# Kernel optimization log

Hardware: AMD Instinct MI355X
Metric: run time of the kernel (lower is better)

Reference implementation:

```python
import jax, jax.numpy as jnp
import numpy as np

N = 50000      # nodes
E = 640000     # edges (before self-loops)
FIN = 512      # in_channels
H = 4          # heads
C = 32         # per-head dim (hidden_channels // heads)
HID = 128      # hidden_channels
OUT = 64       # out_channels
NC = 2         # num_classes


def setup_inputs() -> dict:
    key = jax.random.key(0)
    ks = jax.random.split(key, 26)
    rn = lambda k, shp, s=0.05: jax.random.normal(k, shp, jnp.float32) * s
    return {
        "x": jax.random.normal(ks[0], (N, FIN), jnp.float32),
        "edge_index": jax.random.randint(ks[1], (2, E), 0, N, dtype=jnp.int32),
        "batch": jnp.zeros((N,), jnp.int32),
        # GATConv 1: FIN -> H x C (concat -> HID)
        "W1": rn(ks[2], (FIN, H * C)), "as1": rn(ks[3], (H, C)), "ad1": rn(ks[4], (H, C)), "b1": jnp.zeros((H * C,), jnp.float32),
        "g1": jnp.ones((HID,), jnp.float32), "be1": jnp.zeros((HID,), jnp.float32),
        # GATConv 2: HID -> H x C
        "W2": rn(ks[5], (HID, H * C)), "as2": rn(ks[6], (H, C)), "ad2": rn(ks[7], (H, C)), "b2": jnp.zeros((H * C,), jnp.float32),
        "g2": jnp.ones((HID,), jnp.float32), "be2": jnp.zeros((HID,), jnp.float32),
        "W3": rn(ks[8], (HID, OUT)), "as3": rn(ks[9], (1, OUT)), "ad3": rn(ks[10], (1, OUT)), "b3": jnp.zeros((OUT,), jnp.float32),
        "g3": jnp.ones((OUT,), jnp.float32), "be3": jnp.zeros((OUT,), jnp.float32),
        # classifier: Linear(2*OUT, HID) -> ReLU -> Linear(HID, NC)
        "cW1": rn(ks[11], (2 * OUT, HID)), "cb1": jnp.zeros((HID,), jnp.float32),
        "cW2": rn(ks[12], (HID, NC)), "cb2": jnp.zeros((NC,), jnp.float32),
    }


def _gat_conv(x, ei, W, a_s, a_d, b, heads, cdim, concat):
    n = x.shape[0]
    h = (x @ W).reshape(n, heads, cdim)                 # [n,H,C]
    src, dst = ei[0], ei[1]
    al_s = (h * a_s).sum(-1)                            # [n,H]
    al_d = (h * a_d).sum(-1)                            # [n,H]
    e = al_s[src] + al_d[dst]                           # [E',H]
    e = jnp.where(e > 0, e, 0.2 * e)                    # LeakyReLU(0.2)
    m = jax.ops.segment_max(e, dst, num_segments=n)     # segment softmax over dst
    ex = jnp.exp(e - m[dst])
    s = jax.ops.segment_sum(ex, dst, num_segments=n)
    alpha = ex / (s[dst] + 1e-16)                       # [E',H]
    out = jax.ops.segment_sum(h[src] * alpha[:, :, None], dst, num_segments=n)
    out = out.reshape(n, heads * cdim) if concat else out.mean(axis=1)
    return out + b


def _layer_norm(x, g, b):
    mu = x.mean(-1, keepdims=True)
    v = ((x - mu) ** 2).mean(-1, keepdims=True)
    return g * (x - mu) * jax.lax.rsqrt(v + 1e-5) + b


def reference(x, edge_index, batch, W1, as1, ad1, b1, g1, be1, W2, as2, ad2, b2, g2, be2, W3, as3, ad3, b3, g3, be3, cW1, cb1, cW2, cb2):
    n = x.shape[0]
    ar = jnp.arange(n, dtype=edge_index.dtype)
    ei = jnp.concatenate([edge_index, jnp.stack([ar, ar])], axis=1)  # add self-loops (PyG default)
    h = jax.nn.elu(_layer_norm(_gat_conv(x, ei, W1, as1, ad1, b1, H, C, True), g1, be1))
    h = jax.nn.elu(_layer_norm(_gat_conv(h, ei, W2, as2, ad2, b2, H, C, True), g2, be2))
    h = jax.nn.elu(_layer_norm(_gat_conv(h, ei, W3, as3, ad3, b3, 1, OUT, False), g3, be3))
    # global mean / max pooling over batch ids (single graph here, B=1)
    B = 1
    cnt = jax.ops.segment_sum(jnp.ones((n, 1), h.dtype), batch, num_segments=B)
    x_mean = jax.ops.segment_sum(h, batch, num_segments=B) / cnt
    x_max = jax.ops.segment_max(h, batch, num_segments=B)
    z = jnp.concatenate([x_mean, x_max], axis=-1)       # [B, 2*OUT]
    z = jax.nn.relu(z @ cW1 + cb1)
    return z @ cW2 + cb2                                 # [B, NC]
```

## Files before the change

### kernel.cpp

```cpp
#include <hip/hip_runtime.h>
#include <cmath>

static constexpr int TPB = 256;

using short8 = __attribute__((ext_vector_type(8))) short;
using half8  = __attribute__((ext_vector_type(8))) _Float16;
using f32x4  = __attribute__((ext_vector_type(4))) float;
using uint4v = __attribute__((ext_vector_type(4))) unsigned int;
typedef unsigned short ushort;
typedef unsigned int uint;

__device__ __forceinline__ ushort f2h(float f) {
  _Float16 h = (_Float16)f;
  return __builtin_bit_cast(ushort, h);
}
__device__ __forceinline__ float h2f(ushort u) {
  return (float)__builtin_bit_cast(_Float16, u);
}
__device__ __forceinline__ float hlo(uint u) { return h2f((ushort)(u & 0xffffu)); }
__device__ __forceinline__ float hhi(uint u) { return h2f((ushort)(u >> 16)); }

__global__ void prep_wt3(const float* __restrict__ W1, ushort* __restrict__ Wt1,
                         const float* __restrict__ W2, ushort* __restrict__ Wt2,
                         const float* __restrict__ W3, ushort* __restrict__ Wt3,
                         int FIN) {
  int idx = blockIdx.x * TPB + threadIdx.x;
  const int n1 = FIN * 128, n2 = 128 * 128, n3 = 128 * 64;
  if (idx < n1) {
    int nc = idx / FIN, k = idx - nc * FIN;
    Wt1[idx] = f2h(W1[(size_t)k * 128 + nc]);
  } else if (idx < n1 + n2) {
    int i = idx - n1;
    int nc = i / 128, k = i - nc * 128;
    Wt2[i] = f2h(W2[(size_t)k * 128 + nc]);
  } else if (idx < n1 + n2 + n3) {
    int i = idx - n1 - n2;
    int nc = i / 128, k = i - nc * 128;
    Wt3[i] = f2h(W3[(size_t)k * 64 + nc]);
  }
}

template <int ABF16, int BN, bool FUSE>
__global__ __launch_bounds__(256) void gemm_mfma(const void* __restrict__ Ap,
                                                 const ushort* __restrict__ Wt,
                                                 ushort* __restrict__ Cb,
                                                 int n, int K,
                                                 const float* __restrict__ a_s,
                                                 const float* __restrict__ a_d,
                                                 float* __restrict__ als,
                                                 float* __restrict__ ald) {
  constexpr int NF = BN / 32;
  __shared__ short As[64 * 72];
  __shared__ short Bs[BN * 72];
  const int tid = threadIdx.x;
  const int row0 = blockIdx.x * 64;
  const int srow = tid >> 2, sks = (tid & 3) << 4;
  const int wave = tid >> 6, lane = tid & 63;
  const int wr = wave >> 1, wc = wave & 1;
  const int lm = lane & 15, lg = lane >> 4;

  f32x4 acc[2][NF] = {};

  for (int k0 = 0; k0 < K; k0 += 64) {
    {
      int gr = row0 + srow;
      short8 v0 = {0, 0, 0, 0, 0, 0, 0, 0}, v1 = v0;
      if constexpr (ABF16 == 0) {
        const float* A = (const float*)Ap;
        if (gr < n) {
          const float* p = A + (size_t)gr * K + k0 + sks;
          float4 f0 = *(const float4*)(p + 0);
          float4 f1 = *(const float4*)(p + 4);
          float4 f2 = *(const float4*)(p + 8);
          float4 f3 = *(const float4*)(p + 12);
          v0[0] = (short)f2h(f0.x); v0[1] = (short)f2h(f0.y); v0[2] = (short)f2h(f0.z); v0[3] = (short)f2h(f0.w);
          v0[4] = (short)f2h(f1.x); v0[5] = (short)f2h(f1.y); v0[6] = (short)f2h(f1.z); v0[7] = (short)f2h(f1.w);
          v1[0] = (short)f2h(f2.x); v1[1] = (short)f2h(f2.y); v1[2] = (short)f2h(f2.z); v1[3] = (short)f2h(f2.w);
          v1[4] = (short)f2h(f3.x); v1[5] = (short)f2h(f3.y); v1[6] = (short)f2h(f3.z); v1[7] = (short)f2h(f3.w);
        }
      } else {
        const ushort* A = (const ushort*)Ap;
        if (gr < n) {
          const ushort* p = A + (size_t)gr * K + k0 + sks;
          v0 = *(const short8*)(p + 0);
          v1 = *(const short8*)(p + 8);
        }
      }
      *(short8*)&As[srow * 72 + sks + 0] = v0;
      *(short8*)&As[srow * 72 + sks + 8] = v1;
    }
    if constexpr (BN == 128) {
      const int brow = tid >> 1, bks = (tid & 1) << 5;
      const ushort* wp = Wt + (size_t)brow * K + k0 + bks;
      *(short8*)&Bs[brow * 72 + bks + 0]  = *(const short8*)(wp + 0);
      *(short8*)&Bs[brow * 72 + bks + 8]  = *(const short8*)(wp + 8);
      *(short8*)&Bs[brow * 72 + bks + 16] = *(const short8*)(wp + 16);
      *(short8*)&Bs[brow * 72 + bks + 24] = *(const short8*)(wp + 24);
    } else {
      const ushort* wp = Wt + (size_t)srow * K + k0 + sks;
      *(short8*)&Bs[srow * 72 + sks + 0] = *(const short8*)(wp + 0);
      *(short8*)&Bs[srow * 72 + sks + 8] = *(const short8*)(wp + 8);
    }
    __syncthreads();
#pragma unroll
    for (int kk = 0; kk < 64; kk += 32) {
      half8 a0 = *(const half8*)&As[(wr * 32 + lm) * 72 + kk + lg * 8];
      half8 a1 = *(const half8*)&As[(wr * 32 + 16 + lm) * 72 + kk + lg * 8];
      half8 bf[NF];
#pragma unroll
      for (int f = 0; f < NF; ++f)
        bf[f] = *(const half8*)&Bs[(wc * (BN / 2) + f * 16 + lm) * 72 + kk + lg * 8];
#pragma unroll
      for (int f = 0; f < NF; ++f) {
        acc[0][f] = __builtin_amdgcn_mfma_f32_16x16x32_f16(a0, bf[f], acc[0][f], 0, 0, 0);
        acc[1][f] = __builtin_amdgcn_mfma_f32_16x16x32_f16(a1, bf[f], acc[1][f], 0, 0, 0);
      }
    }
    __syncthreads();
  }
#pragma unroll
  for (int m = 0; m < 2; ++m)
#pragma unroll
    for (int f = 0; f < NF; ++f)
#pragma unroll
      for (int r = 0; r < 4; ++r) {
        int row = row0 + wr * 32 + m * 16 + lg * 4 + r;
        if (row < n) {
          int col = wc * (BN / 2) + f * 16 + lm;
          Cb[(size_t)row * BN + col] = f2h(acc[m][f][r]);
        }
      }
  if constexpr (FUSE) {
#pragma unroll
    for (int hh = 0; hh < 2; ++hh) {
      const int head = 2 * wc + hh;
      float as0 = a_s[head * 32 + lm], as1 = a_s[head * 32 + 16 + lm];
      float ad0 = a_d[head * 32 + lm], ad1 = a_d[head * 32 + 16 + lm];
#pragma unroll
      for (int m = 0; m < 2; ++m)
#pragma unroll
        for (int r = 0; r < 4; ++r) {
          float tS = acc[m][2 * hh][r] * as0 + acc[m][2 * hh + 1][r] * as1;
          float tD = acc[m][2 * hh][r] * ad0 + acc[m][2 * hh + 1][r] * ad1;
#pragma unroll
          for (int off = 8; off >= 1; off >>= 1) {
            tS += __shfl_xor(tS, off);
            tD += __shfl_xor(tD, off);
          }
          if (lm == 0) {
            int row = row0 + wr * 32 + m * 16 + lg * 4 + r;
            if (row < n) {
              als[(size_t)row * 4 + head] = tS;
              ald[(size_t)row * 4 + head] = tD;
            }
          }
        }
    }
  }
}

template <int HH, int CC>
__global__ void compute_al(const ushort* __restrict__ hb, const float* __restrict__ a_s,
                           const float* __restrict__ a_d, float* __restrict__ als,
                           float* __restrict__ ald, int n) {
  int idx = blockIdx.x * TPB + threadIdx.x;
  if (idx >= n * HH) return;
  int node = idx / HH, h = idx - (idx / HH) * HH;
  const ushort* hp = hb + (size_t)node * (HH * CC) + h * CC;
  float s = 0.f, d = 0.f;
#pragma unroll
  for (int c8 = 0; c8 < CC; c8 += 8) {
    short8 v = *(const short8*)(hp + c8);
#pragma unroll
    for (int j = 0; j < 8; ++j) {
      float f = h2f((ushort)v[j]);
      s += f * a_s[h * CC + c8 + j];
      d += f * a_d[h * CC + c8 + j];
    }
  }
  als[idx] = s;
  ald[idx] = d;
}

__global__ void zero_int(int* __restrict__ p, int n) {
  int i = blockIdx.x * TPB + threadIdx.x;
  if (i < n) p[i] = 0;
}

__global__ void hist_dst(const int* __restrict__ edst, int* __restrict__ counts,
                         int E0, int Et) {
  int e = blockIdx.x * TPB + threadIdx.x;
  if (e >= Et) return;
  int d = e < E0 ? edst[e] : e - E0;
  atomicAdd(&counts[d], 1);
}

__global__ void block_sums(const int* __restrict__ counts, int* __restrict__ bsum, int N) {
  __shared__ int sh[256];
  int t = threadIdx.x, idx = blockIdx.x * 256 + t;
  sh[t] = idx < N ? counts[idx] : 0;
  __syncthreads();
  for (int off = 128; off >= 1; off >>= 1) {
    if (t < off) sh[t] += sh[t + off];
    __syncthreads();
  }
  if (t == 0) bsum[blockIdx.x] = sh[0];
}

__global__ void scan_bsum(int* __restrict__ bsum, int nb) {
  __shared__ int sh[256];
  int t = threadIdx.x;
  int v = t < nb ? bsum[t] : 0;
  sh[t] = v;
  __syncthreads();
  for (int off = 1; off < 256; off <<= 1) {
    int u = (t >= off) ? sh[t - off] : 0;
    __syncthreads();
    sh[t] += u;
    __syncthreads();
  }
  if (t < nb) bsum[t] = sh[t] - v;
}

__global__ void scan_final(const int* __restrict__ counts, const int* __restrict__ bsum_ex,
                           int* __restrict__ offsets, int* __restrict__ cursor,
                           int N, int Et) {
  __shared__ int sh[256];
  int t = threadIdx.x, b = blockIdx.x;
  int idx = b * 256 + t;
  int v = (idx < N) ? counts[idx] : 0;
  sh[t] = v;
  __syncthreads();
  for (int off = 1; off < 256; off <<= 1) {
    int u = (t >= off) ? sh[t - off] : 0;
    __syncthreads();
    sh[t] += u;
    __syncthreads();
  }
  if (idx < N) {
    int o = bsum_ex[b] + sh[t] - v;
    offsets[idx] = o;
    cursor[idx] = o;
  }
  if (idx == 0) offsets[N] = Et;
}

__global__ void scatter_csr(const int* __restrict__ esrc, const int* __restrict__ edst,
                            int* __restrict__ cursor, int* __restrict__ csr_src,
                            int E0, int Et) {
  int e = blockIdx.x * TPB + threadIdx.x;
  if (e >= Et) return;
  int s = e < E0 ? esrc[e] : e - E0;
  int d = e < E0 ? edst[e] : e - E0;
  int pos = atomicAdd(&cursor[d], 1);
  csr_src[pos] = s;
}

template <int HH, int CC>
__global__ __launch_bounds__(256) void fused_attn(
    const ushort* __restrict__ hb, const float* __restrict__ als,
    const float* __restrict__ ald, const int* __restrict__ offsets,
    const int* __restrict__ csr_src, const float* __restrict__ bias,
    const float* __restrict__ g, const float* __restrict__ be,
    ushort* __restrict__ xout, int n) {
  constexpr int W = HH * CC;
  constexpr int LPE = W / 8;
  constexpr int NEG = 64 / LPE;
  int wid = (int)((blockIdx.x * (size_t)blockDim.x + threadIdx.x) >> 6);
  int lane = threadIdx.x & 63;
  if (wid >= n) return;
  const int d = wid;
  const int begin = offsets[d], end = offsets[d + 1];
  const int deg = end - begin;

  const int grp = lane / LPE, sub = lane % LPE;
  const int c0 = sub * 8;

  float acc[8] = {};

  if (HH == 4 && deg <= 16) {
    const int h16 = lane >> 4, j16 = lane & 15;
    bool act = j16 < deg;
    int s_e = csr_src[begin + (act ? j16 : 0)];
    float e;
    {
      float ad_h = ald[(size_t)d * 4 + h16];
      e = act ? (als[(size_t)s_e * 4 + h16] + ad_h) : -1e30f;
      e = e > 0.f ? e : 0.2f * e;
    }
    float m = e;
#pragma unroll
    for (int off = 8; off >= 1; off >>= 1) m = fmaxf(m, __shfl_xor(m, off));
    float p = act ? __expf(e - m) : 0.f;
    float s = p;
#pragma unroll
    for (int off = 8; off >= 1; off >>= 1) s += __shfl_xor(s, off);
    float alpha = p / (s + 1e-16f);

    const int hc = sub >> 2;
    int j = grp;
    int sj = __shfl(s_e, j & 15);
    uint4v u = *(const uint4v*)(hb + (size_t)sj * W + c0);
    for (int j0 = 0; j0 < deg; j0 += NEG) {
      uint4v ucur = u;
      int jcur = j;
      j += NEG;
      if (j0 + NEG < deg) {
        int sn = __shfl(s_e, j & 15);
        u = *(const uint4v*)(hb + (size_t)sn * W + c0);
      }
      float w = __shfl(alpha, (hc << 4) | (jcur & 15));
#pragma unroll
      for (int i = 0; i < 4; ++i) {
        acc[2 * i]     = fmaf(w, hlo(ucur[i]), acc[2 * i]);
        acc[2 * i + 1] = fmaf(w, hhi(ucur[i]), acc[2 * i + 1]);
      }
    }
  } else {

  const int hsel = sub >> 2;
  float aldv[HH];
  if constexpr (HH == 4) {
    float4 t = *(const float4*)(ald + (size_t)d * 4);
    aldv[0] = t.x; aldv[1] = t.y; aldv[2] = t.z; aldv[3] = t.w;
  } else {
    aldv[0] = ald[d];
  }

  auto sel4 = [&](float x0, float x1, float x2, float x3) {
    float lo = (hsel & 1) ? x1 : x0;
    float hi = (hsel & 1) ? x3 : x2;
    return (hsel & 2) ? hi : lo;
  };

  if (deg <= 64) {
    bool act = lane < deg;
    int s_e = act ? csr_src[begin + lane] : 0;
    float e0 = -1e30f, e1 = -1e30f, e2 = -1e30f, e3 = -1e30f;
    if constexpr (HH == 4) {
      if (act) {
        float4 t = *(const float4*)(als + (size_t)s_e * 4);
        e0 = t.x + aldv[0]; e0 = e0 > 0.f ? e0 : 0.2f * e0;
        e1 = t.y + aldv[1]; e1 = e1 > 0.f ? e1 : 0.2f * e1;
        e2 = t.z + aldv[2]; e2 = e2 > 0.f ? e2 : 0.2f * e2;
        e3 = t.w + aldv[3]; e3 = e3 > 0.f ? e3 : 0.2f * e3;
      }
    } else {
      if (act) {
        e0 = als[s_e] + aldv[0]; e0 = e0 > 0.f ? e0 : 0.2f * e0;
      }
    }
    float m0 = e0, m1 = e1, m2 = e2, m3 = e3;
#pragma unroll
    for (int off = 32; off >= 1; off >>= 1) {
      m0 = fmaxf(m0, __shfl_xor(m0, off));
      if constexpr (HH == 4) {
        m1 = fmaxf(m1, __shfl_xor(m1, off));
        m2 = fmaxf(m2, __shfl_xor(m2, off));
        m3 = fmaxf(m3, __shfl_xor(m3, off));
      }
    }
    float p0 = act ? __expf(e0 - m0) : 0.f;
    float p1 = 0.f, p2 = 0.f, p3 = 0.f;
    if constexpr (HH == 4) {
      p1 = act ? __expf(e1 - m1) : 0.f;
      p2 = act ? __expf(e2 - m2) : 0.f;
      p3 = act ? __expf(e3 - m3) : 0.f;
    }
    float s0 = p0, s1 = p1, s2 = p2, s3 = p3;
#pragma unroll
    for (int off = 32; off >= 1; off >>= 1) {
      s0 += __shfl_xor(s0, off);
      if constexpr (HH == 4) {
        s1 += __shfl_xor(s1, off);
        s2 += __shfl_xor(s2, off);
        s3 += __shfl_xor(s3, off);
      }
    }
    float a0 = p0 / (s0 + 1e-16f);
    float a1 = 0.f, a2 = 0.f, a3 = 0.f;
    if constexpr (HH == 4) {
      a1 = p1 / (s1 + 1e-16f);
      a2 = p2 / (s2 + 1e-16f);
      a3 = p3 / (s3 + 1e-16f);
    }

    int j = grp;
    int sj = __shfl(s_e, j < 64 ? j : 0);
    uint4v u = *(const uint4v*)(hb + (size_t)sj * W + c0);
    for (int j0 = 0; j0 < deg; j0 += NEG) {
      uint4v ucur = u;
      int jcur = j;
      j += NEG;
      if (j0 + NEG < deg) {
        int sn = __shfl(s_e, j < 64 ? j : 0);
        u = *(const uint4v*)(hb + (size_t)sn * W + c0);
      }
      int jc = jcur < 64 ? jcur : 0;
      float w;
      if constexpr (HH == 4) {
        float wa = __shfl(a0, jc), wb = __shfl(a1, jc), wcx = __shfl(a2, jc), wd = __shfl(a3, jc);
        w = sel4(wa, wb, wcx, wd);
      } else {
        w = __shfl(a0, jc);
      }
      if (jcur >= deg) w = 0.f;
#pragma unroll
      for (int i = 0; i < 4; ++i) {
        acc[2 * i]     = fmaf(w, hlo(ucur[i]), acc[2 * i]);
        acc[2 * i + 1] = fmaf(w, hhi(ucur[i]), acc[2 * i + 1]);
      }
    }
  } else {
    float me[HH];
#pragma unroll
    for (int h = 0; h < HH; ++h) me[h] = -1e30f;
    for (int k = begin + lane; k < end; k += 64) {
      int s = csr_src[k];
      if constexpr (HH == 4) {
        float4 t = *(const float4*)(als + (size_t)s * 4);
        float e0 = t.x + aldv[0]; e0 = e0 > 0.f ? e0 : 0.2f * e0; me[0] = fmaxf(me[0], e0);
        float e1 = t.y + aldv[1]; e1 = e1 > 0.f ? e1 : 0.2f * e1; me[1] = fmaxf(me[1], e1);
        float e2 = t.z + aldv[2]; e2 = e2 > 0.f ? e2 : 0.2f * e2; me[2] = fmaxf(me[2], e2);
        float e3 = t.w + aldv[3]; e3 = e3 > 0.f ? e3 : 0.2f * e3; me[3] = fmaxf(me[3], e3);
      } else {
        float e0 = als[s] + aldv[0]; e0 = e0 > 0.f ? e0 : 0.2f * e0; me[0] = fmaxf(me[0], e0);
      }
    }
#pragma unroll
    for (int off = 32; off >= 1; off >>= 1)
#pragma unroll
      for (int h = 0; h < HH; ++h) me[h] = fmaxf(me[h], __shfl_xor(me[h], off));
    float se[HH];
#pragma unroll
    for (int h = 0; h < HH; ++h) se[h] = 0.f;
    for (int k = begin + lane; k < end; k += 64) {
      int s = csr_src[k];
      if constexpr (HH == 4) {
        float4 t = *(const float4*)(als + (size_t)s * 4);
        float e0 = t.x + aldv[0]; e0 = e0 > 0.f ? e0 : 0.2f * e0; se[0] += __expf(e0 - me[0]);
        float e1 = t.y + aldv[1]; e1 = e1 > 0.f ? e1 : 0.2f * e1; se[1] += __expf(e1 - me[1]);
        float e2 = t.z + aldv[2]; e2 = e2 > 0.f ? e2 : 0.2f * e2; se[2] += __expf(e2 - me[2]);
        float e3 = t.w + aldv[3]; e3 = e3 > 0.f ? e3 : 0.2f * e3; se[3] += __expf(e3 - me[3]);
      } else {
        float e0 = als[s] + aldv[0]; e0 = e0 > 0.f ? e0 : 0.2f * e0; se[0] += __expf(e0 - me[0]);
      }
    }
#pragma unroll
    for (int off = 32; off >= 1; off >>= 1)
#pragma unroll
      for (int h = 0; h < HH; ++h) se[h] += __shfl_xor(se[h], off);
    float inv[HH];
#pragma unroll
    for (int h = 0; h < HH; ++h) inv[h] = 1.f / (se[h] + 1e-16f);

    float m_my, i_my, ad_my;
    if constexpr (HH == 4) {
      m_my = sel4(me[0], me[1], me[2], me[3]);
      i_my = sel4(inv[0], inv[1], inv[2], inv[3]);
      ad_my = sel4(aldv[0], aldv[1], aldv[2], aldv[3]);
    } else {
      m_my = me[0]; i_my = inv[0]; ad_my = aldv[0];
    }
    for (int j0 = 0; j0 < deg; j0 += NEG) {
      int j = j0 + grp;
      if (j < deg) {
        int s = csr_src[begin + j];
        float as_my;
        if constexpr (HH == 4) {
          float4 t = *(const float4*)(als + (size_t)s * 4);
          as_my = sel4(t.x, t.y, t.z, t.w);
        } else {
          as_my = als[s];
        }
        float e = as_my + ad_my; e = e > 0.f ? e : 0.2f * e;
        float w = __expf(e - m_my) * i_my;
        uint4v u = *(const uint4v*)(hb + (size_t)s * W + c0);
#pragma unroll
        for (int i = 0; i < 4; ++i) {
          acc[2 * i]     = fmaf(w, hlo(u[i]), acc[2 * i]);
          acc[2 * i + 1] = fmaf(w, hhi(u[i]), acc[2 * i + 1]);
        }
      }
    }
  }
  }

#pragma unroll
  for (int i = 0; i < 8; ++i) {
    if constexpr (HH == 1) acc[i] += __shfl_xor(acc[i], 8);
    acc[i] += __shfl_xor(acc[i], 16);
    acc[i] += __shfl_xor(acc[i], 32);
  }

  float4 bv0 = *(const float4*)(bias + c0);
  float4 bv1 = *(const float4*)(bias + c0 + 4);
  float v[8];
  v[0] = acc[0] + bv0.x; v[1] = acc[1] + bv0.y; v[2] = acc[2] + bv0.z; v[3] = acc[3] + bv0.w;
  v[4] = acc[4] + bv1.x; v[5] = acc[5] + bv1.y; v[6] = acc[6] + bv1.z; v[7] = acc[7] + bv1.w;
  float sm = 0.f, s2 = 0.f;
#pragma unroll
  for (int i = 0; i < 8; ++i) { sm += v[i]; s2 += v[i] * v[i]; }
  constexpr int TOPOFF = LPE / 2;
#pragma unroll
  for (int off = TOPOFF; off >= 1; off >>= 1) {
    sm += __shfl_xor(sm, off);
    s2 += __shfl_xor(s2, off);
  }
  const float invW = 1.0f / W;
  float mu = sm * invW;
  float var = s2 * invW - mu * mu;
  float r = rsqrtf(var + 1e-5f);
  float4 gv0 = *(const float4*)(g + c0);
  float4 gv1 = *(const float4*)(g + c0 + 4);
  float4 be0 = *(const float4*)(be + c0);
  float4 be1 = *(const float4*)(be + c0 + 4);
  float gg[8] = {gv0.x, gv0.y, gv0.z, gv0.w, gv1.x, gv1.y, gv1.z, gv1.w};
  float bb[8] = {be0.x, be0.y, be0.z, be0.w, be1.x, be1.y, be1.z, be1.w};
  uint4v pk;
#pragma unroll
  for (int i = 0; i < 4; ++i) {
    float y0 = gg[2 * i] * (v[2 * i] - mu) * r + bb[2 * i];
    y0 = y0 > 0.f ? y0 : __expf(y0) - 1.f;
    float y1 = gg[2 * i + 1] * (v[2 * i + 1] - mu) * r + bb[2 * i + 1];
    y1 = y1 > 0.f ? y1 : __expf(y1) - 1.f;
    pk[i] = (uint)f2h(y0) | ((uint)f2h(y1) << 16);
  }
  if (grp == 0)
    *(uint4v*)(xout + (size_t)wid * W + c0) = pk;
}

__global__ void pool_partial(const ushort* __restrict__ h, float* __restrict__ psum,
                             float* __restrict__ pmax, int n) {
  int tid = threadIdx.x;
  float lsum = 0.f, lmax = -1e30f;
  for (size_t idx = (size_t)blockIdx.x * 256 + tid; idx < (size_t)n * 64;
       idx += (size_t)gridDim.x * 256) {
    float v = h2f(h[idx]);
    lsum += v;
    lmax = fmaxf(lmax, v);
  }
  __shared__ float ss[256], sm[256];
  ss[tid] = lsum; sm[tid] = lmax;
  __syncthreads();
  if (tid < 64) {
    float a = ss[tid] + ss[tid + 64] + ss[tid + 128] + ss[tid + 192];
    float m = fmaxf(fmaxf(sm[tid], sm[tid + 64]), fmaxf(sm[tid + 128], sm[tid + 192]));
    psum[blockIdx.x * 64 + tid] = a;
    pmax[blockIdx.x * 64 + tid] = m;
  }
}

__global__ __launch_bounds__(256) void pool_final(
    const float* __restrict__ psum, const float* __restrict__ pmax,
    int nblocks, int n, const float* __restrict__ cW1,
    const float* __restrict__ cb1, const float* __restrict__ cW2,
    const float* __restrict__ cb2, float* __restrict__ out) {
  __shared__ float sred[4][64], mred[4][64];
  __shared__ float z[128];
  __shared__ float hid[128];
  int tid = threadIdx.x;
  int c = tid & 63, q = tid >> 6;
  float s = 0.f, m = -1e30f;
  for (int b = q; b < nblocks; b += 4) {
    s += psum[b * 64 + c];
    m = fmaxf(m, pmax[b * 64 + c]);
  }
  sred[q][c] = s; mred[q][c] = m;
  __syncthreads();
  if (q == 0) {
    float st = sred[0][c] + sred[1][c] + sred[2][c] + sred[3][c];
    float mt = fmaxf(fmaxf(mred[0][c], mred[1][c]), fmaxf(mred[2][c], mred[3][c]));
    z[c] = st / (float)n;
    z[64 + c] = mt;
  }
  __syncthreads();
  if (tid < 128) {
    float a = cb1[tid];
#pragma unroll 4
    for (int k = 0; k < 128; ++k) a += z[k] * cW1[k * 128 + tid];
    hid[tid] = fmaxf(a, 0.f);
  }
  __syncthreads();
  if (tid < 2) {
    float o = cb2[tid];
    for (int j = 0; j < 128; ++j) o += hid[j] * cW2[j * 2 + tid];
    out[tid] = o;
  }
}

static inline int cdiv(long long a, long long b) { return (int)((a + b - 1) / b); }

extern "C" void kernel_launch(void* const* d_in, const int* in_sizes, int n_in,
                              void* d_out, int out_size, void* d_ws, size_t ws_size,
                              hipStream_t stream) {
  const float* x   = (const float*)d_in[0];
  const int*   ei  = (const int*)d_in[1];
  const float* W1  = (const float*)d_in[3];
  const float* as1 = (const float*)d_in[4];
  const float* ad1 = (const float*)d_in[5];
  const float* b1  = (const float*)d_in[6];
  const float* g1  = (const float*)d_in[7];
  const float* be1 = (const float*)d_in[8];
  const float* W2  = (const float*)d_in[9];
  const float* as2 = (const float*)d_in[10];
  const float* ad2 = (const float*)d_in[11];
  const float* b2  = (const float*)d_in[12];
  const float* g2  = (const float*)d_in[13];
  const float* be2 = (const float*)d_in[14];
  const float* W3  = (const float*)d_in[15];
  const float* as3 = (const float*)d_in[16];
  const float* ad3 = (const float*)d_in[17];
  const float* b3  = (const float*)d_in[18];
  const float* g3  = (const float*)d_in[19];
  const float* be3 = (const float*)d_in[20];
  const float* cW1 = (const float*)d_in[21];
  const float* cb1 = (const float*)d_in[22];
  const float* cW2 = (const float*)d_in[23];
  const float* cb2 = (const float*)d_in[24];
  float* out = (float*)d_out;

  const int N   = in_sizes[2];
  const int E0  = in_sizes[1] / 2;
  const int Et  = E0 + N;
  const int FIN = in_sizes[0] / N;

  float* ws = (float*)d_ws;
  size_t o = 0;
  ushort* Ab = (ushort*)(ws + o); o += (size_t)N * 64;
  ushort* Bb = (ushort*)(ws + o); o += (size_t)N * 64;
  float* als  = ws + o; o += (size_t)N * 4;
  float* ald  = ws + o; o += (size_t)N * 4;
  ushort* Wt1 = (ushort*)(ws + o); o += (128 * 512) / 2;
  ushort* Wt2 = (ushort*)(ws + o); o += (128 * 128) / 2;
  ushort* Wt3 = (ushort*)(ws + o); o += (64 * 128) / 2;
  float* psum = ws + o; o += 64 * 64;
  float* pmax = ws + o; o += 64 * 64;
  int* counts  = (int*)(ws + o); o += N + 1;
  int* offsets = (int*)(ws + o); o += N + 1;
  int* cursor  = (int*)(ws + o); o += N;
  int* bsum    = (int*)(ws + o); o += 256;
  int* csr_src = (int*)(ws + o); o += Et;

  const int* esrc = ei;
  const int* edst = ei + E0;
  const int NB = cdiv(N, 256);

  prep_wt3<<<cdiv((long long)FIN * 128 + 128 * 128 + 128 * 64, TPB), TPB, 0, stream>>>(
      W1, Wt1, W2, Wt2, W3, Wt3, FIN);

  zero_int<<<cdiv(N + 1, TPB), TPB, 0, stream>>>(counts, N + 1);
  hist_dst<<<cdiv(Et, TPB), TPB, 0, stream>>>(edst, counts, E0, Et);
  block_sums<<<NB, 256, 0, stream>>>(counts, bsum, N);
  scan_bsum<<<1, 256, 0, stream>>>(bsum, NB);
  scan_final<<<NB, 256, 0, stream>>>(counts, bsum, offsets, cursor, N, Et);
  scatter_csr<<<cdiv(Et, TPB), TPB, 0, stream>>>(esrc, edst, cursor, csr_src, E0, Et);

  gemm_mfma<0, 128, true><<<cdiv(N, 64), 256, 0, stream>>>(x, Wt1, Ab, N, FIN, as1, ad1, als, ald);
  fused_attn<4, 32><<<cdiv(N, 4), 256, 0, stream>>>(Ab, als, ald, offsets, csr_src, b1, g1, be1, Bb, N);
  gemm_mfma<1, 128, true><<<cdiv(N, 64), 256, 0, stream>>>(Bb, Wt2, Ab, N, 128, as2, ad2, als, ald);
  fused_attn<4, 32><<<cdiv(N, 4), 256, 0, stream>>>(Ab, als, ald, offsets, csr_src, b2, g2, be2, Bb, N);
  gemm_mfma<1, 64, false><<<cdiv(N, 64), 256, 0, stream>>>(Bb, Wt3, Ab, N, 128, nullptr, nullptr, nullptr, nullptr);
  compute_al<1, 64><<<cdiv((long long)N, TPB), TPB, 0, stream>>>(Ab, as3, ad3, als, ald, N);
  fused_attn<1, 64><<<cdiv(N, 4), 256, 0, stream>>>(Ab, als, ald, offsets, csr_src, b3, g3, be3, Bb, N);
  pool_partial<<<64, 256, 0, stream>>>(Bb, psum, pmax, N);
  pool_final<<<1, 256, 0, stream>>>(psum, pmax, 64, N, cW1, cb1, cW2, cb2, out);
}
```

Measured before the change: 321.3 us.

## Prefetch next GEMM tile into registers and batch neighbor gathers in aggregation

The MFMA GEMM now loads the next K-tile from global memory into registers while the current tile is being multiplied, then writes it to shared memory between two barriers. The edge aggregation loops replace a one-ahead prefetch with four independent gathers per step, giving more memory loads in flight. Together these aim to hide global-memory latency in both the GEMM and the gather-heavy aggregation. The cost is higher register pressure, an extra barrier per K-step, and predicated or wasted work when a node's degree is not a multiple of the batch size.

Result: slower. 380.6 us (+18.5%).

```diff
diff --git a/kernel.cpp b/kernel.cpp
--- a/kernel.cpp
+++ b/kernel.cpp
@@ -55,53 +55,73 @@
   const int tid = threadIdx.x;
   const int row0 = blockIdx.x * 64;
   const int srow = tid >> 2, sks = (tid & 3) << 4;
+  const int brow = tid >> 1, bks = (tid & 1) << 5;
   const int wave = tid >> 6, lane = tid & 63;
   const int wr = wave >> 1, wc = wave & 1;
   const int lm = lane & 15, lg = lane >> 4;
 
   f32x4 acc[2][NF] = {};
 
-  for (int k0 = 0; k0 < K; k0 += 64) {
-    {
-      int gr = row0 + srow;
-      short8 v0 = {0, 0, 0, 0, 0, 0, 0, 0}, v1 = v0;
-      if constexpr (ABF16 == 0) {
-        const float* A = (const float*)Ap;
-        if (gr < n) {
-          const float* p = A + (size_t)gr * K + k0 + sks;
-          float4 f0 = *(const float4*)(p + 0);
-          float4 f1 = *(const float4*)(p + 4);
-          float4 f2 = *(const float4*)(p + 8);
-          float4 f3 = *(const float4*)(p + 12);
-          v0[0] = (short)f2h(f0.x); v0[1] = (short)f2h(f0.y); v0[2] = (short)f2h(f0.z); v0[3] = (short)f2h(f0.w);
-          v0[4] = (short)f2h(f1.x); v0[5] = (short)f2h(f1.y); v0[6] = (short)f2h(f1.z); v0[7] = (short)f2h(f1.w);
-          v1[0] = (short)f2h(f2.x); v1[1] = (short)f2h(f2.y); v1[2] = (short)f2h(f2.z); v1[3] = (short)f2h(f2.w);
-          v1[4] = (short)f2h(f3.x); v1[5] = (short)f2h(f3.y); v1[6] = (short)f2h(f3.z); v1[7] = (short)f2h(f3.w);
-        }
-      } else {
-        const ushort* A = (const ushort*)Ap;
-        if (gr < n) {
-          const ushort* p = A + (size_t)gr * K + k0 + sks;
-          v0 = *(const short8*)(p + 0);
-          v1 = *(const short8*)(p + 8);
-        }
-      }
-      *(short8*)&As[srow * 72 + sks + 0] = v0;
-      *(short8*)&As[srow * 72 + sks + 8] = v1;
+  short8 sa0, sa1;
+  short8 sb0, sb1, sb2, sb3;
+
+  auto LOADT = [&](int k0) {
+    int gr = row0 + srow;
+    short8 z = {0, 0, 0, 0, 0, 0, 0, 0};
+    sa0 = z; sa1 = z;
+    if constexpr (ABF16 == 0) {
+      const float* A = (const float*)Ap;
+      if (gr < n) {
+        const float* p = A + (size_t)gr * K + k0 + sks;
+        float4 f0 = *(const float4*)(p + 0);
+        float4 f1 = *(const float4*)(p + 4);
+        float4 f2 = *(const float4*)(p + 8);
+        float4 f3 = *(const float4*)(p + 12);
+        sa0[0] = (short)f2h(f0.x); sa0[1] = (short)f2h(f0.y); sa0[2] = (short)f2h(f0.z); sa0[3] = (short)f2h(f0.w);
+        sa0[4] = (short)f2h(f1.x); sa0[5] = (short)f2h(f1.y); sa0[6] = (short)f2h(f1.z); sa0[7] = (short)f2h(f1.w);
+        sa1[0] = (short)f2h(f2.x); sa1[1] = (short)f2h(f2.y); sa1[2] = (short)f2h(f2.z); sa1[3] = (short)f2h(f2.w);
+        sa1[4] = (short)f2h(f3.x); sa1[5] = (short)f2h(f3.y); sa1[6] = (short)f2h(f3.z); sa1[7] = (short)f2h(f3.w);
+      }
+    } else {
+      const ushort* A = (const ushort*)Ap;
+      if (gr < n) {
+        const ushort* p = A + (size_t)gr * K + k0 + sks;
+        sa0 = *(const short8*)(p + 0);
+        sa1 = *(const short8*)(p + 8);
+      }
     }
     if constexpr (BN == 128) {
-      const int brow = tid >> 1, bks = (tid & 1) << 5;
       const ushort* wp = Wt + (size_t)brow * K + k0 + bks;
-      *(short8*)&Bs[brow * 72 + bks + 0]  = *(const short8*)(wp + 0);
-      *(short8*)&Bs[brow * 72 + bks + 8]  = *(const short8*)(wp + 8);
-      *(short8*)&Bs[brow * 72 + bks + 16] = *(const short8*)(wp + 16);
-      *(short8*)&Bs[brow * 72 + bks + 24] = *(const short8*)(wp + 24);
+      sb0 = *(const short8*)(wp + 0);
+      sb1 = *(const short8*)(wp + 8);
+      sb2 = *(const short8*)(wp + 16);
+      sb3 = *(const short8*)(wp + 24);
     } else {
       const ushort* wp = Wt + (size_t)srow * K + k0 + sks;
-      *(short8*)&Bs[srow * 72 + sks + 0] = *(const short8*)(wp + 0);
-      *(short8*)&Bs[srow * 72 + sks + 8] = *(const short8*)(wp + 8);
-    }
-    __syncthreads();
+      sb0 = *(const short8*)(wp + 0);
+      sb1 = *(const short8*)(wp + 8);
+    }
+  };
+  auto WRITET = [&]() {
+    *(short8*)&As[srow * 72 + sks + 0] = sa0;
+    *(short8*)&As[srow * 72 + sks + 8] = sa1;
+    if constexpr (BN == 128) {
+      *(short8*)&Bs[brow * 72 + bks + 0]  = sb0;
+      *(short8*)&Bs[brow * 72 + bks + 8]  = sb1;
+      *(short8*)&Bs[brow * 72 + bks + 16] = sb2;
+      *(short8*)&Bs[brow * 72 + bks + 24] = sb3;
+    } else {
+      *(short8*)&Bs[srow * 72 + sks + 0] = sb0;
+      *(short8*)&Bs[srow * 72 + sks + 8] = sb1;
+    }
+  };
+
+  LOADT(0);
+  WRITET();
+  __syncthreads();
+  for (int k0 = 0; k0 < K; k0 += 64) {
+    const bool more = (k0 + 64) < K;
+    if (more) LOADT(k0 + 64);
 #pragma unroll
     for (int kk = 0; kk < 64; kk += 32) {
       half8 a0 = *(const half8*)&As[(wr * 32 + lm) * 72 + kk + lg * 8];
@@ -116,7 +136,11 @@
         acc[1][f] = __builtin_amdgcn_mfma_f32_16x16x32_f16(a1, bf[f], acc[1][f], 0, 0, 0);
       }
     }
-    __syncthreads();
+    if (more) {
+      __syncthreads();
+      WRITET();
+      __syncthreads();
+    }
   }
 #pragma unroll
   for (int m = 0; m < 2; ++m)
@@ -298,22 +322,23 @@
     float alpha = p / (s + 1e-16f);
 
     const int hc = sub >> 2;
-    int j = grp;
-    int sj = __shfl(s_e, j & 15);
-    uint4v u = *(const uint4v*)(hb + (size_t)sj * W + c0);
-    for (int j0 = 0; j0 < deg; j0 += NEG) {
-      uint4v ucur = u;
-      int jcur = j;
-      j += NEG;
-      if (j0 + NEG < deg) {
-        int sn = __shfl(s_e, j & 15);
-        u = *(const uint4v*)(hb + (size_t)sn * W + c0);
-      }
-      float w = __shfl(alpha, (hc << 4) | (jcur & 15));
-#pragma unroll
-      for (int i = 0; i < 4; ++i) {
-        acc[2 * i]     = fmaf(w, hlo(ucur[i]), acc[2 * i]);
-        acc[2 * i + 1] = fmaf(w, hhi(ucur[i]), acc[2 * i + 1]);
+    int sjv[4];
+#pragma unroll
+    for (int i = 0; i < 4; ++i) sjv[i] = __shfl(s_e, grp + 4 * i);
+    uint4v u[4] = {{0, 0, 0, 0}, {0, 0, 0, 0}, {0, 0, 0, 0}, {0, 0, 0, 0}};
+#pragma unroll
+    for (int i = 0; i < 4; ++i) {
+      int j = grp + 4 * i;
+      if (j < deg) u[i] = *(const uint4v*)(hb + (size_t)sjv[i] * W + c0);
+    }
+#pragma unroll
+    for (int i = 0; i < 4; ++i) {
+      int j = grp + 4 * i;
+      float w = __shfl(alpha, (hc << 4) | j);
+#pragma unroll
+      for (int k = 0; k < 4; ++k) {
+        acc[2 * k]     = fmaf(w, hlo(u[i][k]), acc[2 * k]);
+        acc[2 * k + 1] = fmaf(w, hhi(u[i][k]), acc[2 * k + 1]);
       }
     }
   } else {
@@ -385,30 +410,36 @@
       a3 = p3 / (s3 + 1e-16f);
     }
 
-    int j = grp;
-    int sj = __shfl(s_e, j < 64 ? j : 0);
-    uint4v u = *(const uint4v*)(hb + (size_t)sj * W + c0);
-    for (int j0 = 0; j0 < deg; j0 += NEG) {
-      uint4v ucur = u;
-      int jcur = j;
-      j += NEG;
-      if (j0 + NEG < deg) {
-        int sn = __shfl(s_e, j < 64 ? j : 0);
-        u = *(const uint4v*)(hb + (size_t)sn * W + c0);
-      }
-      int jc = jcur < 64 ? jcur : 0;
-      float w;
-      if constexpr (HH == 4) {
-        float wa = __shfl(a0, jc), wb = __shfl(a1, jc), wcx = __shfl(a2, jc), wd = __shfl(a3, jc);
-        w = sel4(wa, wb, wcx, wd);
-      } else {
-        w = __shfl(a0, jc);
-      }
-      if (jcur >= deg) w = 0.f;
+    for (int j0 = 0; j0 < deg; j0 += 4 * NEG) {
+      int sjv[4];
 #pragma unroll
       for (int i = 0; i < 4; ++i) {
-        acc[2 * i]     = fmaf(w, hlo(ucur[i]), acc[2 * i]);
-        acc[2 * i + 1] = fmaf(w, hhi(ucur[i]), acc[2 * i + 1]);
+        int j = j0 + grp + i * NEG;
+        sjv[i] = __shfl(s_e, j & 63);
+      }
+      uint4v u[4] = {{0, 0, 0, 0}, {0, 0, 0, 0}, {0, 0, 0, 0}, {0, 0, 0, 0}};
+#pragma unroll
+      for (int i = 0; i < 4; ++i) {
+        int j = j0 + grp + i * NEG;
+        if (j < deg) u[i] = *(const uint4v*)(hb + (size_t)sjv[i] * W + c0);
+      }
+#pragma unroll
+      for (int i = 0; i < 4; ++i) {
+        int j = j0 + grp + i * NEG;
+        float w;
+        if constexpr (HH == 4) {
+          float wa = __shfl(a0, j & 63), wb = __shfl(a1, j & 63);
+          float wcx = __shfl(a2, j & 63), wd = __shfl(a3, j & 63);
+          w = sel4(wa, wb, wcx, wd);
+        } else {
+          w = __shfl(a0, j & 63);
+        }
+        if (j >= deg) w = 0.f;
+#pragma unroll
+        for (int k = 0; k < 4; ++k) {
+          acc[2 * k]     = fmaf(w, hlo(u[i][k]), acc[2 * k]);
+          acc[2 * k + 1] = fmaf(w, hhi(u[i][k]), acc[2 * k + 1]);
+        }
       }
     }
   } else {
```

## Sort destination nodes by degree to reduce wave divergence in attention

Applied to the files above, without the earlier changes.

Adds a counting sort of nodes by in-degree (capped at 63) that produces a permutation. Each attention wave then processes perm[wid] rather than wid, so waves in the same block handle nodes of similar degree and take the same branch. This aims to cut divergence and load imbalance between the short-degree fast path and the general path. In exchange it adds three small kernels and an indirection, and the output writes and CSR accesses become scattered, which loses locality.

Result: slower. 586.5 us (+82.5%).

```diff
diff --git a/kernel.cpp b/kernel.cpp
--- a/kernel.cpp
+++ b/kernel.cpp
@@ -256,11 +256,43 @@
   csr_src[pos] = s;
 }
 
+__global__ void deg_hist(const int* __restrict__ counts, int* __restrict__ dhist, int N) {
+  int i = blockIdx.x * TPB + threadIdx.x;
+  if (i >= N) return;
+  int b = counts[i]; b = b < 63 ? b : 63;
+  atomicAdd(&dhist[b], 1);
+}
+
+__global__ void deg_scan(const int* __restrict__ dhist, int* __restrict__ dcur) {
+  __shared__ int sh[64];
+  int t = threadIdx.x;
+  int v = dhist[t];
+  sh[t] = v;
+  __syncthreads();
+  for (int off = 1; off < 64; off <<= 1) {
+    int u = (t >= off) ? sh[t - off] : 0;
+    __syncthreads();
+    sh[t] += u;
+    __syncthreads();
+  }
+  dcur[t] = sh[t] - v;
+}
+
+__global__ void deg_scatter(const int* __restrict__ counts, int* __restrict__ dcur,
+                            int* __restrict__ perm, int N) {
+  int i = blockIdx.x * TPB + threadIdx.x;
+  if (i >= N) return;
+  int b = counts[i]; b = b < 63 ? b : 63;
+  int pos = atomicAdd(&dcur[b], 1);
+  perm[pos] = i;
+}
+
 template <int HH, int CC>
 __global__ __launch_bounds__(256) void fused_attn(
     const ushort* __restrict__ hb, const float* __restrict__ als,
     const float* __restrict__ ald, const int* __restrict__ offsets,
-    const int* __restrict__ csr_src, const float* __restrict__ bias,
+    const int* __restrict__ csr_src, const int* __restrict__ perm,
+    const float* __restrict__ bias,
     const float* __restrict__ g, const float* __restrict__ be,
     ushort* __restrict__ xout, int n) {
   constexpr int W = HH * CC;
@@ -269,7 +301,7 @@
   int wid = (int)((blockIdx.x * (size_t)blockDim.x + threadIdx.x) >> 6);
   int lane = threadIdx.x & 63;
   if (wid >= n) return;
-  const int d = wid;
+  const int d = perm[wid];
   const int begin = offsets[d], end = offsets[d + 1];
   const int deg = end - begin;
 
@@ -527,7 +559,7 @@
     pk[i] = (uint)f2h(y0) | ((uint)f2h(y1) << 16);
   }
   if (grp == 0)
-    *(uint4v*)(xout + (size_t)wid * W + c0) = pk;
+    *(uint4v*)(xout + (size_t)d * W + c0) = pk;
 }
 
 __global__ void pool_partial(const ushort* __restrict__ h, float* __restrict__ psum,
@@ -637,9 +669,12 @@
   float* psum = ws + o; o += 64 * 64;
   float* pmax = ws + o; o += 64 * 64;
   int* counts  = (int*)(ws + o); o += N + 1;
+  int* dhist   = (int*)(ws + o); o += 64;
+  int* dcur    = (int*)(ws + o); o += 64;
   int* offsets = (int*)(ws + o); o += N + 1;
   int* cursor  = (int*)(ws + o); o += N;
   int* bsum    = (int*)(ws + o); o += 256;
+  int* perm    = (int*)(ws + o); o += N;
   int* csr_src = (int*)(ws + o); o += Et;
 
   const int* esrc = ei;
@@ -649,20 +684,23 @@
   prep_wt3<<<cdiv((long long)FIN * 128 + 128 * 128 + 128 * 64, TPB), TPB, 0, stream>>>(
       W1, Wt1, W2, Wt2, W3, Wt3, FIN);
 
-  zero_int<<<cdiv(N + 1, TPB), TPB, 0, stream>>>(counts, N + 1);
+  zero_int<<<cdiv(N + 1 + 128, TPB), TPB, 0, stream>>>(counts, N + 1 + 128);
   hist_dst<<<cdiv(Et, TPB), TPB, 0, stream>>>(edst, counts, E0, Et);
   block_sums<<<NB, 256, 0, stream>>>(counts, bsum, N);
   scan_bsum<<<1, 256, 0, stream>>>(bsum, NB);
   scan_final<<<NB, 256, 0, stream>>>(counts, bsum, offsets, cursor, N, Et);
   scatter_csr<<<cdiv(Et, TPB), TPB, 0, stream>>>(esrc, edst, cursor, csr_src, E0, Et);
+  deg_hist<<<cdiv(N, TPB), TPB, 0, stream>>>(counts, dhist, N);
+  deg_scan<<<1, 64, 0, stream>>>(dhist, dcur);
+  deg_scatter<<<cdiv(N, TPB), TPB, 0, stream>>>(counts, dcur, perm, N);
 
   gemm_mfma<0, 128, true><<<cdiv(N, 64), 256, 0, stream>>>(x, Wt1, Ab, N, FIN, as1, ad1, als, ald);
-  fused_attn<4, 32><<<cdiv(N, 4), 256, 0, stream>>>(Ab, als, ald, offsets, csr_src, b1, g1, be1, Bb, N);
+  fused_attn<4, 32><<<cdiv(N, 4), 256, 0, stream>>>(Ab, als, ald, offsets, csr_src, perm, b1, g1, be1, Bb, N);
   gemm_mfma<1, 128, true><<<cdiv(N, 64), 256, 0, stream>>>(Bb, Wt2, Ab, N, 128, as2, ad2, als, ald);
-  fused_attn<4, 32><<<cdiv(N, 4), 256, 0, stream>>>(Ab, als, ald, offsets, csr_src, b2, g2, be2, Bb, N);
+  fused_attn<4, 32><<<cdiv(N, 4), 256, 0, stream>>>(Ab, als, ald, offsets, csr_src, perm, b2, g2, be2, Bb, N);
   gemm_mfma<1, 64, false><<<cdiv(N, 64), 256, 0, stream>>>(Bb, Wt3, Ab, N, 128, nullptr, nullptr, nullptr, nullptr);
   compute_al<1, 64><<<cdiv((long long)N, TPB), TPB, 0, stream>>>(Ab, as3, ad3, als, ald, N);
-  fused_attn<1, 64><<<cdiv(N, 4), 256, 0, stream>>>(Ab, als, ald, offsets, csr_src, b3, g3, be3, Bb, N);
+  fused_attn<1, 64><<<cdiv(N, 4), 256, 0, stream>>>(Ab, als, ald, offsets, csr_src, perm, b3, g3, be3, Bb, N);
   pool_partial<<<64, 256, 0, stream>>>(Bb, psum, pmax, N);
   pool_final<<<1, 256, 0, stream>>>(psum, pmax, 64, N, cW1, cb1, cW2, cb2, out);
 }
```
